# Kernel tuning notes

Hardware: AMD Instinct MI355X
Metric: run time of the kernel (lower is better)

The kernel has to match this reference:

```python
import jax, jax.numpy as jnp
import numpy as np

D_MODEL = 768
NUM_HEADS = 12
D_K = D_MODEL // NUM_HEADS


def setup_inputs() -> dict:
    key = jax.random.key(0)
    ks = jax.random.split(key, 11)
    B, S = 2, 2048
    sc = 1.0 / np.sqrt(D_MODEL)
    return {
        "q": jax.random.normal(ks[0], (B, S, D_MODEL), jnp.float32),
        "k": jax.random.normal(ks[1], (B, S, D_MODEL), jnp.float32),
        "v": jax.random.normal(ks[2], (B, S, D_MODEL), jnp.float32),
        "w_q": jax.random.normal(ks[3], (D_MODEL, D_MODEL), jnp.float32) * sc,
        "b_q": jnp.zeros((D_MODEL,), jnp.float32),
        "w_k": jax.random.normal(ks[4], (D_MODEL, D_MODEL), jnp.float32) * sc,
        "b_k": jnp.zeros((D_MODEL,), jnp.float32),
        "w_v": jax.random.normal(ks[5], (D_MODEL, D_MODEL), jnp.float32) * sc,
        "b_v": jnp.zeros((D_MODEL,), jnp.float32),
        "w_o": jax.random.normal(ks[6], (D_MODEL, D_MODEL), jnp.float32) * sc,
        "b_o": jnp.zeros((D_MODEL,), jnp.float32),
    }


def _split_heads(x, B):
    # [B, S, D] -> [B, H, S, d_k]
    return x.reshape(B, -1, NUM_HEADS, D_K).transpose(0, 2, 1, 3)


def reference(q, k, v, w_q, b_q, w_k, b_k, w_v, b_v, w_o, b_o):
    B = q.shape[0]
    # torch nn.Linear: y = x @ W.T + b; weights stored [out, in]
    qh = _split_heads(q @ w_q.T + b_q, B)
    kh = _split_heads(k @ w_k.T + b_k, B)
    vh = _split_heads(v @ w_v.T + b_v, B)
    scores = jnp.einsum("bhsd,bhtd->bhst", qh, kh) / jnp.sqrt(jnp.float32(D_K))
    attn = jax.nn.softmax(scores, axis=-1)
    ctx = jnp.einsum("bhst,bhtd->bhsd", attn, vh)
    ctx = ctx.transpose(0, 2, 1, 3).reshape(B, -1, D_MODEL)
    return ctx @ w_o.T + b_o
```

## Files before the change

### kernel.cpp

```cpp
#include <hip/hip_runtime.h>
#include <cstdint>


#define S_LEN 2048
#define NHEAD 12
#define DMODEL 768

typedef short s16x8 __attribute__((ext_vector_type(8)));
typedef float f32x4 __attribute__((ext_vector_type(4)));

#define MFMA16(a, b, c) __builtin_amdgcn_mfma_f32_16x16x32_bf16((a), (b), (c), 0, 0, 0)

__device__ __forceinline__ void lds_dma16(void* lds, const void* g) {
  __builtin_amdgcn_global_load_lds(
      (const __attribute__((address_space(1))) unsigned int*)g,
      (__attribute__((address_space(3))) unsigned int*)lds, 16, 0, 0);
}

__device__ __forceinline__ unsigned int pk_bf16(float a, float b) {
  unsigned int ua = __float_as_uint(a), ub = __float_as_uint(b);
  ua = (ua + 0x7FFFu + ((ua >> 16) & 1u)) >> 16;
  ub = (ub + 0x7FFFu + ((ub >> 16) & 1u)) >> 16;
  return ua | (ub << 16);
}
__device__ __forceinline__ short bf16r(float a) {
  unsigned int ua = __float_as_uint(a);
  return (short)((ua + 0x7FFFu + ((ua >> 16) & 1u)) >> 16);
}
__device__ __forceinline__ unsigned int pk_trunc(float a, float b) {
  return __builtin_amdgcn_perm(__float_as_uint(b), __float_as_uint(a), 0x07060302u);
}
__device__ __forceinline__ float bf16_floor(float a) {
  return __uint_as_float(__float_as_uint(a) & 0xFFFF0000u);
}

__global__ __launch_bounds__(256)
void convert_all(const float* __restrict__ q, const float* __restrict__ k,
                 const float* __restrict__ v,
                 const float* __restrict__ w0, const float* __restrict__ w1,
                 const float* __restrict__ w2, const float* __restrict__ w3,
                 short* __restrict__ qb, short* __restrict__ kb,
                 short* __restrict__ vb,
                 short* __restrict__ o0, short* __restrict__ o1,
                 short* __restrict__ o2, short* __restrict__ o3) {
  int b = blockIdx.x;
  const float* src;
  short* dst;
  if (b < 9216) {
    const int s = b / 3072;
    src = (s == 0) ? q : (s == 1) ? k : v;
    dst = (s == 0) ? qb : (s == 1) ? kb : vb;
    b -= s * 3072;
  } else {
    b -= 9216;
    const int s = b / 576;
    src = (s == 0) ? w0 : (s == 1) ? w1 : (s == 2) ? w2 : w3;
    dst = (s == 0) ? o0 : (s == 1) ? o1 : (s == 2) ? o2 : o3;
    b -= s * 576;
  }
  const long i = ((long)b * 256 + threadIdx.x) * 4;
  float4 f = *(const float4*)(src + i);
  uint2 u;
  u.x = pk_bf16(f.x, f.y);
  u.y = pk_bf16(f.z, f.w);
  *(uint2*)(dst + i) = u;
}

__global__ __launch_bounds__(256)
void qkv_kernel(const short* __restrict__ qb, const short* __restrict__ kb,
                const short* __restrict__ vb,
                const short* __restrict__ wq, const short* __restrict__ wk,
                const short* __restrict__ wv,
                const float* __restrict__ bq, const float* __restrict__ bk,
                const float* __restrict__ bv,
                short* __restrict__ qh, short* __restrict__ kh,
                short* __restrict__ vt) {
  constexpr int K = 768;
  __shared__ short Abuf[128 * 32];
  __shared__ short Bbuf[128 * 32];

  const int L   = blockIdx.x;
  const int xcd = L & 7;
  const int i   = L >> 3;
  const int nt  = i % 6;
  const int pl  = xcd * 12 + i / 6;
  const int z   = pl >> 5;
  const int mt  = pl & 31;
  const int m0  = mt * 128;
  const int n0  = nt * 128;

  const short* A = (z == 0) ? qb : (z == 1) ? kb : vb;
  const short* B = (z == 0) ? wq : (z == 1) ? wk : wv;
  const float* bias = (z == 0) ? bq : (z == 1) ? bk : bv;

  const int tid  = threadIdx.x;
  const int lane = tid & 63;
  const int w    = tid >> 6;
  const int g    = lane >> 4;
  const int c    = lane & 15;
  const int wm   = (w & 1) * 64;
  const int wn   = (w >> 1) * 64;

  const int drow = w * 32 + (lane >> 2);
  const int dcol = (lane & 3) * 8;
  const short* Ag = A + (long)(m0 + drow) * K + dcol;
  const short* Bg = B + (long)(n0 + drow) * K + dcol;
  short* Al0 = &Abuf[w * 1024];
  short* Al1 = &Abuf[w * 1024 + 512];
  short* Bl0 = &Bbuf[w * 1024];
  short* Bl1 = &Bbuf[w * 1024 + 512];

  f32x4 acc[4][4];
#pragma unroll
  for (int a = 0; a < 4; ++a)
#pragma unroll
    for (int b2 = 0; b2 < 4; ++b2) acc[a][b2] = (f32x4){0.f, 0.f, 0.f, 0.f};

  for (int kt = 0; kt < K; kt += 32) {
    lds_dma16(Al0, Ag + kt);
    lds_dma16(Al1, Ag + (long)16 * K + kt);
    lds_dma16(Bl0, Bg + kt);
    lds_dma16(Bl1, Bg + (long)16 * K + kt);
    __syncthreads();

    s16x8 af[4], bf[4];
#pragma unroll
    for (int mb = 0; mb < 4; ++mb)
      af[mb] = *(const s16x8*)&Abuf[(wm + mb * 16 + c) * 32 + g * 8];
#pragma unroll
    for (int nb = 0; nb < 4; ++nb)
      bf[nb] = *(const s16x8*)&Bbuf[(wn + nb * 16 + c) * 32 + g * 8];
#pragma unroll
    for (int mb = 0; mb < 4; ++mb)
#pragma unroll
      for (int nb = 0; nb < 4; ++nb)
        acc[mb][nb] = MFMA16(af[mb], bf[nb], acc[mb][nb]);
    __syncthreads();
  }

  if (z < 2) {
    short* outp = z ? kh : qh;
    const float scale = z ? 1.0f : 0.18033688011112042f;
#pragma unroll
    for (int mb = 0; mb < 4; ++mb) {
#pragma unroll
      for (int nb = 0; nb < 4; ++nb) {
        const int n = n0 + wn + nb * 16 + c;
        const float bvv = bias[n];
        const int hh = n >> 6, d = n & 63;
#pragma unroll
        for (int r = 0; r < 4; ++r) {
          const int m = m0 + wm + mb * 16 + g * 4 + r;
          const int b2 = m >> 11, s = m & 2047;
          const float val = (acc[mb][nb][r] + bvv) * scale;
          outp[(((long)(b2 * NHEAD + hh) * S_LEN + s) << 6) + d] = bf16r(val);
        }
      }
    }
  } else {
#pragma unroll
    for (int mb = 0; mb < 4; ++mb) {
#pragma unroll
      for (int nb = 0; nb < 4; ++nb) {
        const int n = n0 + wn + nb * 16 + c;
        const float bvv = bias[n];
        const int hh = n >> 6, d = n & 63;
        const int m_base = m0 + wm + mb * 16 + g * 4;
        const int b2 = m_base >> 11, t = m_base & 2047;
        uint2 ov;
        ov.x = pk_bf16(acc[mb][nb][0] + bvv, acc[mb][nb][1] + bvv);
        ov.y = pk_bf16(acc[mb][nb][2] + bvv, acc[mb][nb][3] + bvv);
        *(uint2*)(vt + ((long)(b2 * NHEAD + hh) * 64 + d) * S_LEN + t) = ov;
      }
    }
  }
}

__global__ __launch_bounds__(256)
void o_kernel(const short* __restrict__ ctx, const short* __restrict__ wo,
              const float* __restrict__ bo, float* __restrict__ out) {
  constexpr int K = 768;
  __shared__ short Abuf[64 * 32];
  __shared__ short Bbuf[128 * 32];

  const int L   = blockIdx.x;
  const int xcd = L & 7;
  const int i   = L >> 3;
  const int nt  = i % 6;
  const int mt  = xcd * 8 + i / 6;
  const int m0  = mt * 64;
  const int n0  = nt * 128;

  const int tid  = threadIdx.x;
  const int lane = tid & 63;
  const int w    = tid >> 6;
  const int g    = lane >> 4;
  const int c    = lane & 15;
  const int wm   = (w & 1) * 32;
  const int wn   = (w >> 1) * 64;

  const int arow = w * 16 + (lane >> 2);
  const int brow = w * 32 + (lane >> 2);
  const int dcol = (lane & 3) * 8;
  const short* Ag = ctx + (long)(m0 + arow) * K + dcol;
  const short* Bg = wo + (long)(n0 + brow) * K + dcol;
  short* Al = &Abuf[w * 512];
  short* Bl0 = &Bbuf[w * 1024];
  short* Bl1 = &Bbuf[w * 1024 + 512];

  f32x4 acc[2][4];
#pragma unroll
  for (int a = 0; a < 2; ++a)
#pragma unroll
    for (int b2 = 0; b2 < 4; ++b2) acc[a][b2] = (f32x4){0.f, 0.f, 0.f, 0.f};

  for (int kt = 0; kt < K; kt += 32) {
    lds_dma16(Al, Ag + kt);
    lds_dma16(Bl0, Bg + kt);
    lds_dma16(Bl1, Bg + (long)16 * K + kt);
    __syncthreads();

    s16x8 af[2], bf[4];
#pragma unroll
    for (int mb = 0; mb < 2; ++mb)
      af[mb] = *(const s16x8*)&Abuf[(wm + mb * 16 + c) * 32 + g * 8];
#pragma unroll
    for (int nb = 0; nb < 4; ++nb)
      bf[nb] = *(const s16x8*)&Bbuf[(wn + nb * 16 + c) * 32 + g * 8];
#pragma unroll
    for (int mb = 0; mb < 2; ++mb)
#pragma unroll
      for (int nb = 0; nb < 4; ++nb)
        acc[mb][nb] = MFMA16(af[mb], bf[nb], acc[mb][nb]);
    __syncthreads();
  }

#pragma unroll
  for (int mb = 0; mb < 2; ++mb) {
#pragma unroll
    for (int nb = 0; nb < 4; ++nb) {
      const int n = n0 + wn + nb * 16 + c;
      const float bvv = bo[n];
#pragma unroll
      for (int r = 0; r < 4; ++r) {
        const int m = m0 + wm + mb * 16 + g * 4 + r;
        out[(long)m * DMODEL + n] = acc[mb][nb][r] + bvv;
      }
    }
  }
}

__global__ __launch_bounds__(256)
void attn_kernel(const short* __restrict__ Qh, const short* __restrict__ Kh,
                 const short* __restrict__ Vt, short* __restrict__ Ctx) {
  __shared__ short kbuf[2][64 * 64];
  __shared__ short vbuf[2][64 * 64];
  __shared__ short pbuf[4][16 * 64];

  const int tid  = threadIdx.x;
  const int lane = tid & 63;
  const int w    = tid >> 6;
  const int g    = lane >> 4;
  const int c    = lane & 15;
  const int bh   = blockIdx.y;
  const int qs0  = blockIdx.x * 64;
  const long base = (long)bh * S_LEN * 64;
  const short* Qb = Qh + base;
  const short* Kb = Kh + base;
  const short* Vb = Vt + base;

  const long qrow = (long)(qs0 + w * 16 + c) * 64;
  const s16x8 qf0 = *(const s16x8*)(Qb + qrow + g * 8);
  const s16x8 qf1 = *(const s16x8*)(Qb + qrow + 32 + g * 8);

  f32x4 co[4];
#pragma unroll
  for (int i = 0; i < 4; ++i) co[i] = (f32x4){0.f, 0.f, 0.f, 0.f};
  float l_lane = 0.f;

  const int srow = tid >> 2;
  const int sq   = tid & 3;
  const int sw   = srow & 7;
  const int sg0  = ((2 * sq)     ^ sw) * 8;
  const int sg1  = ((2 * sq + 1) ^ sw) * 8;
  const int cw   = c & 7;
  const int rg0  = ((g)     ^ cw) * 8;
  const int rg1  = ((4 + g) ^ cw) * 8;

  const short* kg = Kb + (long)srow * 64 + sq * 16;
  const short* vg = Vb + (long)srow * S_LEN + sq * 16;

  uint4 rkA0, rkA1, rvA0, rvA1;
  uint4 rkB0, rkB1, rvB0, rvB1;
  auto fetchA = [&](long t0) {
    rkA0 = *(const uint4*)(kg + t0 * 64);
    rkA1 = *(const uint4*)(kg + t0 * 64 + 8);
    rvA0 = *(const uint4*)(vg + t0);
    rvA1 = *(const uint4*)(vg + t0 + 8);
  };
  auto fetchB = [&](long t0) {
    rkB0 = *(const uint4*)(kg + t0 * 64);
    rkB1 = *(const uint4*)(kg + t0 * 64 + 8);
    rvB0 = *(const uint4*)(vg + t0);
    rvB1 = *(const uint4*)(vg + t0 + 8);
  };
  auto storeA = [&](short* kb2, short* vb2) {
    *(uint4*)&kb2[srow * 64 + sg0] = rkA0;
    *(uint4*)&kb2[srow * 64 + sg1] = rkA1;
    *(uint4*)&vb2[srow * 64 + sg0] = rvA0;
    *(uint4*)&vb2[srow * 64 + sg1] = rvA1;
  };
  auto storeB = [&](short* kb2, short* vb2) {
    *(uint4*)&kb2[srow * 64 + sg0] = rkB0;
    *(uint4*)&kb2[srow * 64 + sg1] = rkB1;
    *(uint4*)&vb2[srow * 64 + sg0] = rvB0;
    *(uint4*)&vb2[srow * 64 + sg1] = rvB1;
  };

  const int pr0 = c * 64 + ((g ^ cw) * 8);
  const int pr1 = c * 64 + (((4 + g) ^ cw) * 8);

  auto step = [&](const short* kb2, const short* vb2) {
    f32x4 st[4];
#pragma unroll
    for (int mb = 0; mb < 4; ++mb) {
      const s16x8 k0 = *(const s16x8*)&kb2[(mb * 16 + c) * 64 + rg0];
      const s16x8 k1 = *(const s16x8*)&kb2[(mb * 16 + c) * 64 + rg1];
      f32x4 z = (f32x4){0.f, 0.f, 0.f, 0.f};
      z = MFMA16(k0, qf0, z);
      z = MFMA16(k1, qf1, z);
      st[mb] = z;
    }
#pragma unroll
    for (int mb = 0; mb < 4; ++mb) {
      float p0 = __builtin_amdgcn_exp2f(st[mb][0]);
      float p1 = __builtin_amdgcn_exp2f(st[mb][1]);
      float p2 = __builtin_amdgcn_exp2f(st[mb][2]);
      float p3 = __builtin_amdgcn_exp2f(st[mb][3]);
      l_lane += bf16_floor(p0) + bf16_floor(p1) + bf16_floor(p2) + bf16_floor(p3);
      uint2 pw;
      pw.x = pk_trunc(p0, p1);
      pw.y = pk_trunc(p2, p3);
      const int pg = ((2 * mb + (g >> 1)) ^ cw) * 8 + (g & 1) * 4;
      *(uint2*)&pbuf[w][c * 64 + pg] = pw;
    }
    const s16x8 pb0 = *(const s16x8*)&pbuf[w][pr0];
    const s16x8 pb1 = *(const s16x8*)&pbuf[w][pr1];
#pragma unroll
    for (int db = 0; db < 4; ++db) {
      const s16x8 v0 = *(const s16x8*)&vb2[(db * 16 + c) * 64 + rg0];
      const s16x8 v1 = *(const s16x8*)&vb2[(db * 16 + c) * 64 + rg1];
      co[db] = MFMA16(v0, pb0, co[db]);
      co[db] = MFMA16(v1, pb1, co[db]);
    }
  };

  constexpr int NT = S_LEN / 64;
  fetchA(0);
  fetchB(64);
  storeA(kbuf[0], vbuf[0]);
  for (int j = 0; j < NT / 2; ++j) {
    __syncthreads();
    fetchA((2 * j + 2 < NT) ? (long)(2 * j + 2) * 64 : 0);
    step(kbuf[0], vbuf[0]);
    storeB(kbuf[1], vbuf[1]);
    __syncthreads();
    fetchB((2 * j + 3 < NT) ? (long)(2 * j + 3) * 64 : 0);
    step(kbuf[1], vbuf[1]);
    storeA(kbuf[0], vbuf[0]);
  }

  float rs = l_lane;
  rs += __shfl_xor(rs, 16);
  rs += __shfl_xor(rs, 32);
  const float invl = 1.f / rs;

  const int hh = bh % NHEAD;
  const long tok = (long)(bh / NHEAD) * S_LEN + qs0 + w * 16 + c;
#pragma unroll
  for (int db = 0; db < 4; ++db) {
    uint2 ov;
    ov.x = pk_bf16(co[db][0] * invl, co[db][1] * invl);
    ov.y = pk_bf16(co[db][2] * invl, co[db][3] * invl);
    *(uint2*)(Ctx + tok * DMODEL + hh * 64 + db * 16 + g * 4) = ov;
  }
}

extern "C" void kernel_launch(void* const* d_in, const int* in_sizes, int n_in,
                              void* d_out, int out_size, void* d_ws, size_t ws_size,
                              hipStream_t stream) {
  const float* q   = (const float*)d_in[0];
  const float* k   = (const float*)d_in[1];
  const float* v   = (const float*)d_in[2];
  const float* w_q = (const float*)d_in[3];
  const float* b_q = (const float*)d_in[4];
  const float* w_k = (const float*)d_in[5];
  const float* b_k = (const float*)d_in[6];
  const float* w_v = (const float*)d_in[7];
  const float* b_v = (const float*)d_in[8];
  const float* w_o = (const float*)d_in[9];
  const float* b_o = (const float*)d_in[10];
  float* out = (float*)d_out;

  const long NELEM = (long)2 * NHEAD * S_LEN * 64;
  const long WELEM = (long)DMODEL * DMODEL;
  short* qh  = (short*)d_ws;
  short* kh  = qh + NELEM;
  short* vt  = kh + NELEM;
  short* wqb = vt + NELEM;
  short* wkb = wqb + WELEM;
  short* wvb = wkb + WELEM;
  short* wob = wvb + WELEM;
  short* qb  = wob + WELEM;
  short* kb  = qb + NELEM;
  short* vb  = kb + NELEM;
  short* ctx = qb;

  dim3 blk(256);
  convert_all<<<dim3(11520), blk, 0, stream>>>(q, k, v, w_q, w_k, w_v, w_o,
                                               qb, kb, vb, wqb, wkb, wvb, wob);
  qkv_kernel<<<dim3(576), blk, 0, stream>>>(qb, kb, vb, wqb, wkb, wvb,
                                            b_q, b_k, b_v, qh, kh, vt);
  attn_kernel<<<dim3(32, 24), blk, 0, stream>>>(qh, kh, vt, ctx);
  o_kernel<<<dim3(384), blk, 0, stream>>>(ctx, wob, b_o, out);
}
```

Baseline: 203.2 us.

## Load V fragments directly from global memory instead of staging through LDS

The attention kernel no longer copies V tiles into a double-buffered shared-memory array. Each wave now reads its V MFMA operands straight from global memory at the start of every step, and raises wave priority around the PV MFMA block. This removes the V LDS stores and reads, halves the kernel's LDS footprint, and frees registers that held the V prefetch. In exchange, every wave fetches the whole V tile, so global/L2 traffic for V is four times higher. Those loads are row-strided and only partly hidden behind the QK^T compute.

```diff
diff --git a/kernel.cpp b/kernel.cpp
--- a/kernel.cpp
+++ b/kernel.cpp
@@ -254,7 +254,6 @@
 void attn_kernel(const short* __restrict__ Qh, const short* __restrict__ Kh,
                  const short* __restrict__ Vt, short* __restrict__ Ctx) {
   __shared__ short kbuf[2][64 * 64];
-  __shared__ short vbuf[2][64 * 64];
   __shared__ short pbuf[4][16 * 64];
 
   const int tid  = threadIdx.x;
@@ -288,39 +287,38 @@
   const int rg1  = ((4 + g) ^ cw) * 8;
 
   const short* kg = Kb + (long)srow * 64 + sq * 16;
-  const short* vg = Vb + (long)srow * S_LEN + sq * 16;
-
-  uint4 rkA0, rkA1, rvA0, rvA1;
-  uint4 rkB0, rkB1, rvB0, rvB1;
+  const short* vbase = Vb + (long)c * S_LEN + g * 8;
+
+  uint4 rkA0, rkA1;
+  uint4 rkB0, rkB1;
   auto fetchA = [&](long t0) {
     rkA0 = *(const uint4*)(kg + t0 * 64);
     rkA1 = *(const uint4*)(kg + t0 * 64 + 8);
-    rvA0 = *(const uint4*)(vg + t0);
-    rvA1 = *(const uint4*)(vg + t0 + 8);
   };
   auto fetchB = [&](long t0) {
     rkB0 = *(const uint4*)(kg + t0 * 64);
     rkB1 = *(const uint4*)(kg + t0 * 64 + 8);
-    rvB0 = *(const uint4*)(vg + t0);
-    rvB1 = *(const uint4*)(vg + t0 + 8);
   };
-  auto storeA = [&](short* kb2, short* vb2) {
+  auto storeA = [&](short* kb2) {
     *(uint4*)&kb2[srow * 64 + sg0] = rkA0;
     *(uint4*)&kb2[srow * 64 + sg1] = rkA1;
-    *(uint4*)&vb2[srow * 64 + sg0] = rvA0;
-    *(uint4*)&vb2[srow * 64 + sg1] = rvA1;
   };
-  auto storeB = [&](short* kb2, short* vb2) {
+  auto storeB = [&](short* kb2) {
     *(uint4*)&kb2[srow * 64 + sg0] = rkB0;
     *(uint4*)&kb2[srow * 64 + sg1] = rkB1;
-    *(uint4*)&vb2[srow * 64 + sg0] = rvB0;
-    *(uint4*)&vb2[srow * 64 + sg1] = rvB1;
   };
 
   const int pr0 = c * 64 + ((g ^ cw) * 8);
   const int pr1 = c * 64 + (((4 + g) ^ cw) * 8);
 
-  auto step = [&](const short* kb2, const short* vb2) {
+  auto step = [&](const short* kb2, long t0) {
+    s16x8 vf0[4], vf1[4];
+#pragma unroll
+    for (int db = 0; db < 4; ++db) {
+      const short* vp = vbase + (long)db * 16 * S_LEN + t0;
+      vf0[db] = *(const s16x8*)vp;
+      vf1[db] = *(const s16x8*)(vp + 32);
+    }
     f32x4 st[4];
 #pragma unroll
     for (int mb = 0; mb < 4; ++mb) {
@@ -346,28 +344,28 @@
     }
     const s16x8 pb0 = *(const s16x8*)&pbuf[w][pr0];
     const s16x8 pb1 = *(const s16x8*)&pbuf[w][pr1];
+    __builtin_amdgcn_s_setprio(1);
 #pragma unroll
     for (int db = 0; db < 4; ++db) {
-      const s16x8 v0 = *(const s16x8*)&vb2[(db * 16 + c) * 64 + rg0];
-      const s16x8 v1 = *(const s16x8*)&vb2[(db * 16 + c) * 64 + rg1];
-      co[db] = MFMA16(v0, pb0, co[db]);
-      co[db] = MFMA16(v1, pb1, co[db]);
-    }
+      co[db] = MFMA16(vf0[db], pb0, co[db]);
+      co[db] = MFMA16(vf1[db], pb1, co[db]);
+    }
+    __builtin_amdgcn_s_setprio(0);
   };
 
   constexpr int NT = S_LEN / 64;
   fetchA(0);
   fetchB(64);
-  storeA(kbuf[0], vbuf[0]);
+  storeA(kbuf[0]);
   for (int j = 0; j < NT / 2; ++j) {
     __syncthreads();
     fetchA((2 * j + 2 < NT) ? (long)(2 * j + 2) * 64 : 0);
-    step(kbuf[0], vbuf[0]);
-    storeB(kbuf[1], vbuf[1]);
+    step(kbuf[0], (long)(2 * j) * 64);
+    storeB(kbuf[1]);
     __syncthreads();
     fetchB((2 * j + 3 < NT) ? (long)(2 * j + 3) * 64 : 0);
-    step(kbuf[1], vbuf[1]);
-    storeA(kbuf[0], vbuf[0]);
+    step(kbuf[1], (long)(2 * j + 1) * 64);
+    storeA(kbuf[0]);
   }
 
   float rs = l_lane;
```

Result: slower. 254.3 us (+25.1%).

## Stream K/V tiles into LDS via direct global-to-LDS DMA with double buffering

Applied to the files above, without the earlier changes.

Replaces the register-staged K/V tile loads and LDS stores in the attention kernel with global_load_lds DMA writes straight into a double-buffered LDS ring. A tile two steps ahead is prefetched, with vmcnt waits and barriers guarding reuse. This removes VGPR staging and ds_write traffic, keeping the XOR swizzle by permuting the source addresses. MFMA priority is also raised around the PV accumulation. The risk is that the hand-placed waitcnt and barriers expose DMA latency or a subtle race on buffer reuse.

```diff
diff --git a/kernel.cpp b/kernel.cpp
--- a/kernel.cpp
+++ b/kernel.cpp
@@ -278,45 +278,22 @@
   for (int i = 0; i < 4; ++i) co[i] = (f32x4){0.f, 0.f, 0.f, 0.f};
   float l_lane = 0.f;
 
-  const int srow = tid >> 2;
-  const int sq   = tid & 3;
-  const int sw   = srow & 7;
-  const int sg0  = ((2 * sq)     ^ sw) * 8;
-  const int sg1  = ((2 * sq + 1) ^ sw) * 8;
+  const int drow  = w * 8 + (lane >> 3);
+  const int dchk  = ((lane & 7) ^ (lane >> 3)) * 8;
+  const short* kdma = Kb + (long)drow * 64 + dchk;
+  const short* vdma = Vb + (long)drow * S_LEN + dchk;
+
+  auto dma_tile = [&](int p, long t0) {
+#pragma unroll
+    for (int i = 0; i < 2; ++i) {
+      lds_dma16(&kbuf[p][(i * 32 + w * 8) * 64], kdma + (t0 + i * 32) * 64);
+      lds_dma16(&vbuf[p][(i * 32 + w * 8) * 64], vdma + (long)i * 32 * S_LEN + t0);
+    }
+  };
+
   const int cw   = c & 7;
   const int rg0  = ((g)     ^ cw) * 8;
   const int rg1  = ((4 + g) ^ cw) * 8;
-
-  const short* kg = Kb + (long)srow * 64 + sq * 16;
-  const short* vg = Vb + (long)srow * S_LEN + sq * 16;
-
-  uint4 rkA0, rkA1, rvA0, rvA1;
-  uint4 rkB0, rkB1, rvB0, rvB1;
-  auto fetchA = [&](long t0) {
-    rkA0 = *(const uint4*)(kg + t0 * 64);
-    rkA1 = *(const uint4*)(kg + t0 * 64 + 8);
-    rvA0 = *(const uint4*)(vg + t0);
-    rvA1 = *(const uint4*)(vg + t0 + 8);
-  };
-  auto fetchB = [&](long t0) {
-    rkB0 = *(const uint4*)(kg + t0 * 64);
-    rkB1 = *(const uint4*)(kg + t0 * 64 + 8);
-    rvB0 = *(const uint4*)(vg + t0);
-    rvB1 = *(const uint4*)(vg + t0 + 8);
-  };
-  auto storeA = [&](short* kb2, short* vb2) {
-    *(uint4*)&kb2[srow * 64 + sg0] = rkA0;
-    *(uint4*)&kb2[srow * 64 + sg1] = rkA1;
-    *(uint4*)&vb2[srow * 64 + sg0] = rvA0;
-    *(uint4*)&vb2[srow * 64 + sg1] = rvA1;
-  };
-  auto storeB = [&](short* kb2, short* vb2) {
-    *(uint4*)&kb2[srow * 64 + sg0] = rkB0;
-    *(uint4*)&kb2[srow * 64 + sg1] = rkB1;
-    *(uint4*)&vb2[srow * 64 + sg0] = rvB0;
-    *(uint4*)&vb2[srow * 64 + sg1] = rvB1;
-  };
-
   const int pr0 = c * 64 + ((g ^ cw) * 8);
   const int pr1 = c * 64 + (((4 + g) ^ cw) * 8);
 
@@ -350,24 +327,26 @@
     for (int db = 0; db < 4; ++db) {
       const s16x8 v0 = *(const s16x8*)&vb2[(db * 16 + c) * 64 + rg0];
       const s16x8 v1 = *(const s16x8*)&vb2[(db * 16 + c) * 64 + rg1];
+      __builtin_amdgcn_s_setprio(1);
       co[db] = MFMA16(v0, pb0, co[db]);
       co[db] = MFMA16(v1, pb1, co[db]);
+      __builtin_amdgcn_s_setprio(0);
     }
   };
 
   constexpr int NT = S_LEN / 64;
-  fetchA(0);
-  fetchB(64);
-  storeA(kbuf[0], vbuf[0]);
-  for (int j = 0; j < NT / 2; ++j) {
-    __syncthreads();
-    fetchA((2 * j + 2 < NT) ? (long)(2 * j + 2) * 64 : 0);
-    step(kbuf[0], vbuf[0]);
-    storeB(kbuf[1], vbuf[1]);
-    __syncthreads();
-    fetchB((2 * j + 3 < NT) ? (long)(2 * j + 3) * 64 : 0);
-    step(kbuf[1], vbuf[1]);
-    storeA(kbuf[0], vbuf[0]);
+  dma_tile(0, 0);
+  dma_tile(1, 64);
+  int p = 0;
+  for (int j = 0; j < NT; ++j) {
+    asm volatile("s_waitcnt vmcnt(4)" ::: "memory");
+    __builtin_amdgcn_s_barrier();
+    __builtin_amdgcn_sched_barrier(0);
+    step(kbuf[p], vbuf[p]);
+    __builtin_amdgcn_s_barrier();
+    const long tn = (j + 2 < NT) ? (long)(j + 2) * 64 : 0;
+    dma_tile(p, tn);
+    p ^= 1;
   }
 
   float rs = l_lane;
```

New measurement: 204.7 us. Within noise of the previous version (+0.7%).
